# Kernel tuning notes

Hardware: AMD Instinct MI355X
Metric: run time of the kernel (lower is better)

## Reference

```python
import jax, jax.numpy as jnp
import numpy as np

NU, NT, E, H = 100000, 200000, 1000000, 64
NUM_LAYERS = 3


def setup_inputs() -> dict:
    key = jax.random.key(0)
    ks = jax.random.split(key, 16)
    s = 0.05
    inp = {}
    inp["x_user"] = jax.random.normal(ks[0], (NU, 32), jnp.float32)
    inp["x_transaction"] = jax.random.normal(ks[1], (NT, 64), jnp.float32)
    inp["ei_u2u"] = jax.random.randint(ks[2], (2, E), 0, NU, jnp.int32)
    inp["ei_t2t"] = jax.random.randint(ks[3], (2, E), 0, NT, jnp.int32)
    inp["ei_u2t"] = jnp.stack([jax.random.randint(ks[4], (E,), 0, NU),
                               jax.random.randint(ks[5], (E,), 0, NT)]).astype(jnp.int32)
    inp["ei_t2u"] = jnp.stack([jax.random.randint(ks[6], (E,), 0, NT),
                               jax.random.randint(ks[7], (E,), 0, NU)]).astype(jnp.int32)
    inp["W_emb_user"] = jax.random.normal(ks[8], (32, H), jnp.float32) * s
    inp["b_emb_user"] = jnp.zeros((H,), jnp.float32)
    inp["W_emb_txn"] = jax.random.normal(ks[9], (64, H), jnp.float32) * s
    inp["b_emb_txn"] = jnp.zeros((H,), jnp.float32)
    # one GCNConv weight/bias per (layer, edge_type): order u2u, t2t, u2t, t2u
    inp["conv_W"] = jax.random.normal(ks[10], (NUM_LAYERS, 4, H, H), jnp.float32) * s
    inp["conv_b"] = jnp.zeros((NUM_LAYERS, 4, H), jnp.float32)
    inp["W1"] = jax.random.normal(ks[11], (H, H), jnp.float32) * s
    inp["b1"] = jnp.zeros((H,), jnp.float32)
    inp["W2"] = jax.random.normal(ks[12], (H, 1), jnp.float32) * s
    inp["b2"] = jnp.zeros((1,), jnp.float32)
    return inp


def _gcn(h_src, ei, n_src, n_dst, W, b, self_loops):
    """GCNConv: x W with symmetric degree normalization, scatter-sum into dst."""
    src, dst = ei[0], ei[1]
    if self_loops:  # same node type on both ends: add self loops (PyG default)
        loop = jnp.arange(n_dst, dtype=src.dtype)
        src = jnp.concatenate([src, loop])
        dst = jnp.concatenate([dst, loop])
        deg = jax.ops.segment_sum(jnp.ones_like(dst, jnp.float32), dst, num_segments=n_dst)
        dinv = jnp.where(deg > 0, jax.lax.rsqrt(jnp.maximum(deg, 1.0)), 0.0)
        norm = dinv[src] * dinv[dst]
    else:  # bipartite relation: out-degree of src, in-degree of dst
        ds = jax.ops.segment_sum(jnp.ones_like(src, jnp.float32), src, num_segments=n_src)
        dd = jax.ops.segment_sum(jnp.ones_like(dst, jnp.float32), dst, num_segments=n_dst)
        dsi = jnp.where(ds > 0, jax.lax.rsqrt(jnp.maximum(ds, 1.0)), 0.0)
        ddi = jnp.where(dd > 0, jax.lax.rsqrt(jnp.maximum(dd, 1.0)), 0.0)
        norm = dsi[src] * ddi[dst]
    m = h_src @ W  # [N_src, H] transform first (GCNConv order)
    out = jax.ops.segment_sum(m[src] * norm[:, None], dst, num_segments=n_dst)
    return out + b


def reference(x_user, x_transaction, ei_u2u, ei_t2t, ei_u2t, ei_t2u,
              W_emb_user, b_emb_user, W_emb_txn, b_emb_txn,
              conv_W, conv_b, W1, b1, W2, b2):
    hu = x_user @ W_emb_user + b_emb_user          # [NU, H]
    ht = x_transaction @ W_emb_txn + b_emb_txn     # [NT, H]
    for l in range(NUM_LAYERS):
        ou1 = _gcn(hu, ei_u2u, NU, NU, conv_W[l, 0], conv_b[l, 0], True)
        ot1 = _gcn(ht, ei_t2t, NT, NT, conv_W[l, 1], conv_b[l, 1], True)
        ot2 = _gcn(hu, ei_u2t, NU, NT, conv_W[l, 2], conv_b[l, 2], False)
        ou2 = _gcn(ht, ei_t2u, NT, NU, conv_W[l, 3], conv_b[l, 3], False)
        # HeteroConv aggr='mean' across relations per dst type, then ReLU
        hu = jax.nn.relu((ou1 + ou2) * 0.5)
        ht = jax.nn.relu((ot1 + ot2) * 0.5)
    g = jnp.stack([hu.mean(axis=0), ht.mean(axis=0)])  # [2, H] per-type global mean
    x = g.mean(axis=0, keepdims=True)                  # [1, H]
    x = jax.nn.relu(x @ W1 + b1)                       # dropout is identity at eval
    return jax.nn.sigmoid(x @ W2 + b2)                 # [1, 1]
```

## Files before the change

### kernel.cpp

```cpp
#include <hip/hip_runtime.h>
#include <hip/hip_bf16.h>
#include <hip/hip_fp8.h>

#define NU_ 100000
#define NT_ 200000
#define NE_ 1000000
#define HD  64
#define NL  3

#define OFF0 0
#define OFF1 (NU_)
#define OFF2 (NU_ + NT_)
#define OFF3 (NU_ + 2 * NT_)
#define OFF4 (2 * NU_ + 2 * NT_)
#define OFF5 (3 * NU_ + 2 * NT_)
#define HTOT (3 * NU_ + 3 * NT_)
#define RPT2 (NU_ + NT_)

#define NBU 391
#define NBT 782
#define NBTOT2 (NBU + NBT)

#define PB1  512
#define BKP  2048
#define NBKC 147
#define NBKS 147
#define NBKT (NBKC + NBKS)

#define WPK_EMBU 0
#define WPK_EMBT 2048
#define WPK_CONV 6144
#define WPK_TOT  55296

#define EMU 512
#define EMT 1024
#define GMU 512
#define GMT 1024
#define GBU 3125
#define GBT 6250

typedef float floatx2 __attribute__((ext_vector_type(2)));
typedef _Float16 f16x8 __attribute__((ext_vector_type(8)));
typedef float f32x4 __attribute__((ext_vector_type(4)));
typedef unsigned short u16x8 __attribute__((ext_vector_type(8)));

__device__ __forceinline__ unsigned char enc_fp8(float v) {
    return (unsigned char)__hip_cvt_float_to_fp8(v, __HIP_SATFINITE, __HIP_E4M3);
}

__device__ __forceinline__ float dec1_fp8(unsigned int u) {
    int e = (u >> 3) & 15;
    int m = u & 7;
    int mant = m | (e ? 8 : 0);
    if (u & 0x80) mant = -mant;
    int ex = (e ? e : 1) - 10;
    return (float)mant * __uint_as_float((unsigned int)(ex + 127) << 23);
}

__device__ __forceinline__ void dec4_fp8(unsigned int u, float* f) {
#if __has_builtin(__builtin_amdgcn_cvt_pk_f32_fp8)
    floatx2 lo = __builtin_amdgcn_cvt_pk_f32_fp8((int)u, false);
    floatx2 hi = __builtin_amdgcn_cvt_pk_f32_fp8((int)u, true);
    f[0] = lo.x; f[1] = lo.y; f[2] = hi.x; f[3] = hi.y;
#else
    f[0] = dec1_fp8(u & 0xff);
    f[1] = dec1_fp8((u >> 8) & 0xff);
    f[2] = dec1_fp8((u >> 16) & 0xff);
    f[3] = dec1_fp8((u >> 24) & 0xff);
#endif
}

__global__ void detect_dtype(const unsigned short* __restrict__ x, int* __restrict__ flag, int n) {
    __shared__ int s_big;
    if (threadIdx.x == 0) s_big = 0;
    __syncthreads();
    int big = 0;
    for (int i = threadIdx.x; i < n; i += blockDim.x) {
        float v = __uint_as_float(((unsigned int)x[i]) << 16);
        if (!(fabsf(v) < 1.0e4f)) big = 1;
    }
    if (big) atomicAdd(&s_big, 1);
    __syncthreads();
    if (threadIdx.x == 0) flag[0] = (s_big > 0) ? 0 : 1;
}

struct Ptr10 { const void* p[10]; };

__global__ void cvt_weights(Ptr10 src, float* __restrict__ dst, float* __restrict__ gsum,
                            const int* __restrict__ flag) {
    const int c[11] = {0, 2048, 2112, 6208, 6272, 55424, 56192, 60288, 60352, 60416, 60417};
    int i = blockIdx.x * blockDim.x + threadIdx.x;
    if (i < 64) gsum[i] = 0.f;
    if (i >= 60417) return;
    int r = 0;
#pragma unroll
    for (int k = 1; k < 10; ++k)
        if (i >= c[k]) r = k;
    int e = i - c[r];
    if (flag[0]) {
        unsigned short u = ((const unsigned short*)src.p[r])[e];
        dst[i] = __uint_as_float(((unsigned int)u) << 16);
    } else {
        dst[i] = ((const float*)src.p[r])[e];
    }
}

__global__ void pack_weights(const float* __restrict__ wts, _Float16* __restrict__ wpk) {
    int gid = blockIdx.x * 256 + threadIdx.x;
    if (gid >= WPK_TOT) return;
    const float* W;
    int r, KS;
    if (gid < WPK_EMBT) { W = wts; r = gid; KS = 1; }
    else if (gid < WPK_CONV) { W = wts + 2112; r = gid - WPK_EMBT; KS = 2; }
    else {
        int mat = (gid - WPK_CONV) >> 12;
        W = wts + 6272 + mat * 4096;
        r = (gid - WPK_CONV) & 4095;
        KS = 2;
    }
    int j = r & 7;
    int lane = (r >> 3) & 63;
    int f = r >> 9;
    int ct = f / KS;
    int s = f - ct * KS;
    int k = 32 * s + 8 * (lane >> 4) + j;
    int n = 16 * ct + (lane & 15);
    wpk[gid] = (_Float16)W[k * 64 + n];
}

__device__ __forceinline__ void p1_dev(int bid, const int* __restrict__ eu2u,
                                       const int* __restrict__ et2t,
                                       const int* __restrict__ eu2t,
                                       const int* __restrict__ et2u,
                                       int* __restrict__ gcnt, int* __restrict__ bofs) {
    __shared__ int cnt[NBKT];
    for (int j = threadIdx.x; j < NBKT; j += 256) cnt[j] = 0;
    __syncthreads();
    for (int i = bid * 256 + threadIdx.x; i < 6 * NE_; i += PB1 * 256) {
        int b;
        if (i < 4 * NE_) {
            int m;
            if (i < NE_)          m = eu2u[i + NE_];
            else if (i < 2 * NE_) m = NU_ + et2t[i];
            else if (i < 3 * NE_) m = NU_ + eu2t[i - NE_];
            else                  m = et2u[i - 2 * NE_];
            b = m >> 11;
        } else {
            int m2 = (i < 5 * NE_) ? eu2t[i - 4 * NE_] : (NU_ + et2u[i - 5 * NE_]);
            b = NBKC + (m2 >> 11);
        }
        atomicAdd(&cnt[b], 1);
    }
    __syncthreads();
    for (int j = threadIdx.x; j < NBKT; j += 256) {
        bofs[bid * NBKT + j] = atomicAdd(&gcnt[j], cnt[j]);
    }
}

template <int K>
__device__ __forceinline__ void embed_mfma_dev(int t0, int tstride, int ntiles,
                                               const void* __restrict__ x,
                                               const _Float16* __restrict__ Wpk,
                                               const float* __restrict__ bias,
                                               _Float16* __restrict__ out,
                                               const int* __restrict__ flag) {
    constexpr int KS = K / 32;
    const int lane = threadIdx.x & 63;
    const int rq = lane & 15;
    const int oct = lane >> 4;

    f16x8 bf[4][KS];
#pragma unroll
    for (int ct = 0; ct < 4; ++ct)
#pragma unroll
        for (int s = 0; s < KS; ++s)
            bf[ct][s] = *(const f16x8*)(Wpk + (((ct * KS + s) << 9) + (lane << 3)));
    float bv[4];
#pragma unroll
    for (int ct = 0; ct < 4; ++ct) bv[ct] = bias[16 * ct + rq];

    const bool isb = flag[0] != 0;

    for (int t = t0; t < ntiles; t += tstride) {
        const int r0 = t << 4;
        f16x8 a[KS];
        if (isb) {
            const unsigned short* xr = (const unsigned short*)x + (size_t)(r0 + rq) * K + 8 * oct;
#pragma unroll
            for (int s = 0; s < KS; ++s) {
                u16x8 uv = *(const u16x8*)(xr + 32 * s);
                f16x8 v;
#pragma unroll
                for (int j = 0; j < 8; ++j)
                    v[j] = (_Float16)__uint_as_float(((unsigned int)uv[j]) << 16);
                a[s] = v;
            }
        } else {
            const float* xr = (const float*)x + (size_t)(r0 + rq) * K + 8 * oct;
#pragma unroll
            for (int s = 0; s < KS; ++s) {
                float4 x0 = *(const float4*)(xr + 32 * s);
                float4 x1 = *(const float4*)(xr + 32 * s + 4);
                f16x8 v;
                v[0] = (_Float16)x0.x; v[1] = (_Float16)x0.y;
                v[2] = (_Float16)x0.z; v[3] = (_Float16)x0.w;
                v[4] = (_Float16)x1.x; v[5] = (_Float16)x1.y;
                v[6] = (_Float16)x1.z; v[7] = (_Float16)x1.w;
                a[s] = v;
            }
        }

        f32x4 acc[4];
#pragma unroll
        for (int ct = 0; ct < 4; ++ct) acc[ct] = (f32x4){0.f, 0.f, 0.f, 0.f};
#pragma unroll
        for (int ct = 0; ct < 4; ++ct)
#pragma unroll
            for (int s = 0; s < KS; ++s)
                acc[ct] = __builtin_amdgcn_mfma_f32_16x16x32_f16(a[s], bf[ct][s], acc[ct], 0, 0, 0);

        const int rb = r0 + (oct << 2);
#pragma unroll
        for (int ct = 0; ct < 4; ++ct)
#pragma unroll
            for (int g = 0; g < 4; ++g)
                out[(size_t)(rb + g) * HD + 16 * ct + rq] = (_Float16)(acc[ct][g] + bv[ct]);
    }
}

__global__ __launch_bounds__(256) void fused_p1_embed(
    const int* __restrict__ eu2u, const int* __restrict__ et2t,
    const int* __restrict__ eu2t, const int* __restrict__ et2u,
    int* __restrict__ gcnt, int* __restrict__ bofs,
    const void* __restrict__ x_user, const void* __restrict__ x_txn,
    const _Float16* __restrict__ wpk,
    const float* __restrict__ bembu, const float* __restrict__ bembt,
    _Float16* __restrict__ hu, _Float16* __restrict__ ht, const int* __restrict__ flag) {
    int b = blockIdx.x;
    int wid = threadIdx.x >> 6;
    if (b < PB1) {
        p1_dev(b, eu2u, et2t, eu2t, et2u, gcnt, bofs);
    } else if (b < PB1 + EMU) {
        embed_mfma_dev<32>((b - PB1) * 4 + wid, EMU * 4, NU_ / 16, x_user,
                           wpk + WPK_EMBU, bembu, hu, flag);
    } else {
        embed_mfma_dev<64>((b - PB1 - EMU) * 4 + wid, EMT * 4, NT_ / 16, x_txn,
                           wpk + WPK_EMBT, bembt, ht, flag);
    }
}

__global__ __launch_bounds__(256) void p2_scatter(
    const int* __restrict__ eu2u, const int* __restrict__ et2t,
    const int* __restrict__ eu2t, const int* __restrict__ et2u,
    const int* __restrict__ gcnt, int* __restrict__ gbase, const int* __restrict__ bofs,
    unsigned int* __restrict__ part_csr, unsigned int* __restrict__ part_src) {
    __shared__ int gb[NBKT];
    __shared__ int lofs[NBKT];
    const int t = threadIdx.x;
    for (int j = t; j < NBKT; j += 256) { lofs[j] = 0; gb[j] = gcnt[j]; }
    __syncthreads();
    if (t == 0) {
        int s = 0;
        for (int j = 0; j < NBKC; ++j) { int c = gb[j]; gb[j] = s; s += c; }
        s = 0;
        for (int j = NBKC; j < NBKT; ++j) { int c = gb[j]; gb[j] = s; s += c; }
    }
    __syncthreads();
    const int bid = blockIdx.x;
    if (bid == 0)
        for (int j = t; j < NBKT; j += 256) gbase[j] = gb[j];
    for (int i = bid * 256 + t; i < 6 * NE_; i += PB1 * 256) {
        if (i < 4 * NE_) {
            int m; unsigned int src, tag;
            if (i < NE_)          { m = eu2u[i + NE_];        src = (unsigned int)eu2u[i];           tag = 0u; }
            else if (i < 2 * NE_) { m = NU_ + et2t[i];        src = (unsigned int)et2t[i - NE_];     tag = 1u; tag = 0u; }
            else if (i < 3 * NE_) { m = NU_ + eu2t[i - NE_];  src = (unsigned int)eu2t[i - 2 * NE_]; tag = 1u; }
            else                  { m = et2u[i - 2 * NE_];    src = (unsigned int)et2u[i - 3 * NE_]; tag = 1u; }
            int b = m >> 11;
            int l = atomicAdd(&lofs[b], 1);
            int pos = gb[b] + bofs[bid * NBKT + b] + l;
            part_csr[pos] = (src << 12) | (tag << 11) | (unsigned int)(m & (BKP - 1));
        } else {
            int m2 = (i < 5 * NE_) ? eu2t[i - 4 * NE_] : (NU_ + et2u[i - 5 * NE_]);
            int b = NBKC + (m2 >> 11);
            int l = atomicAdd(&lofs[b], 1);
            int pos = gb[b] + bofs[bid * NBKT + b] + l;
            part_src[pos] = (unsigned int)m2;
        }
    }
}

__global__ __launch_bounds__(1024) void bucket_count(const unsigned int* __restrict__ part_csr,
                                                     const unsigned int* __restrict__ part_src,
                                                     const int* __restrict__ gcnt,
                                                     const int* __restrict__ gbase,
                                                     int* __restrict__ hist) {
    __shared__ int cA[BKP];
    __shared__ int cB[BKP];
    const int b = blockIdx.x;
    const int n = gcnt[b];
    const int base = gbase[b];
    const int t = threadIdx.x;
    for (int j = t; j < BKP; j += 1024) { cA[j] = 0; cB[j] = 0; }
    __syncthreads();
    if (b < NBKC) {
        for (int i = t; i < n; i += 1024) {
            unsigned int it = part_csr[base + i];
            int l = (int)(it & (BKP - 1));
            if (it & 0x800u) atomicAdd(&cB[l], 1);
            else             atomicAdd(&cA[l], 1);
        }
        __syncthreads();
        const int m0 = b << 11;
        for (int j = t; j < BKP; j += 1024) {
            int m = m0 + j;
            if (m < NU_ + NT_) {
                int oA = (m < NU_) ? (OFF0 + m) : (OFF1 + (m - NU_));
                int oB = (m < NU_) ? (OFF3 + m) : (OFF2 + (m - NU_));
                hist[oA] = cA[j];
                hist[oB] = cB[j];
            }
        }
    } else {
        for (int i = t; i < n; i += 1024) {
            unsigned int m2 = part_src[base + i];
            atomicAdd(&cA[(int)(m2 & (BKP - 1))], 1);
        }
        __syncthreads();
        const int m0 = (b - NBKC) << 11;
        for (int j = t; j < BKP; j += 1024) {
            int m2 = m0 + j;
            if (m2 < NU_ + NT_) {
                int o = (m2 < NU_) ? (OFF4 + m2) : (OFF5 + (m2 - NU_));
                hist[o] = cA[j];
            }
        }
    }
}

__global__ __launch_bounds__(1024) void bucket_place(const unsigned int* __restrict__ part_csr,
                                                     const int* __restrict__ gcnt,
                                                     const int* __restrict__ gbase,
                                                     const int* __restrict__ rp,
                                                     int* __restrict__ colU,
                                                     int* __restrict__ colT) {
    __shared__ int fl[BKP];
    const int b = blockIdx.x;
    const int n = gcnt[b];
    const int base = gbase[b];
    const int t = threadIdx.x;
    for (int j = t; j < BKP; j += 1024) fl[j] = 0;
    __syncthreads();
    const int m0 = b << 11;
    for (int i = t; i < n; i += 1024) {
        unsigned int it = part_csr[base + i];
        int mlow = (int)(it & (BKP - 1));
        int m = m0 + mlow;
        int ofs = atomicAdd(&fl[mlow], 1);
        int colv = (int)(((it >> 12) << 6) | ((it & 0x800u) << 20));
        if (m < NU_) colU[rp[m] + ofs] = colv;
        else         colT[rp[m] + ofs] = colv;
    }
}

__device__ __forceinline__ void gemm_mfma_dev(int t0, int tstride, int ntiles,
                                              const _Float16* __restrict__ h,
                                              const _Float16* __restrict__ WApk,
                                              const _Float16* __restrict__ WBpk,
                                              const float* __restrict__ scA,
                                              const float* __restrict__ scB,
                                              unsigned char* __restrict__ mA,
                                              unsigned char* __restrict__ mB) {
    const int lane = threadIdx.x & 63;
    const int rq = lane & 15;
    const int oct = lane >> 4;

    f16x8 bf[2][4][2];
#pragma unroll
    for (int m = 0; m < 2; ++m) {
        const _Float16* P = m ? WBpk : WApk;
#pragma unroll
        for (int ct = 0; ct < 4; ++ct)
#pragma unroll
            for (int s = 0; s < 2; ++s)
                bf[m][ct][s] = *(const f16x8*)(P + ((((ct << 1) + s) << 9) + (lane << 3)));
    }

    for (int t = t0; t < ntiles; t += tstride) {
        const int r0 = t << 4;
        const _Float16* hr = h + (size_t)(r0 + rq) * HD + 8 * oct;
        f16x8 a0 = *(const f16x8*)(hr);
        f16x8 a1 = *(const f16x8*)(hr + 32);

        f32x4 acc[2][4];
#pragma unroll
        for (int m = 0; m < 2; ++m)
#pragma unroll
            for (int ct = 0; ct < 4; ++ct) acc[m][ct] = (f32x4){0.f, 0.f, 0.f, 0.f};

#pragma unroll
        for (int m = 0; m < 2; ++m)
#pragma unroll
            for (int ct = 0; ct < 4; ++ct) {
                acc[m][ct] = __builtin_amdgcn_mfma_f32_16x16x32_f16(a0, bf[m][ct][0],
                                                                   acc[m][ct], 0, 0, 0);
                acc[m][ct] = __builtin_amdgcn_mfma_f32_16x16x32_f16(a1, bf[m][ct][1],
                                                                   acc[m][ct], 0, 0, 0);
            }

        const int rb = r0 + (oct << 2);
        float sa[4], sb[4];
#pragma unroll
        for (int g = 0; g < 4; ++g) { sa[g] = scA[rb + g]; sb[g] = scB[rb + g]; }
#pragma unroll
        for (int ct = 0; ct < 4; ++ct)
#pragma unroll
            for (int g = 0; g < 4; ++g) {
                mA[(size_t)(rb + g) * HD + 16 * ct + rq] = enc_fp8(acc[0][ct][g] * sa[g]);
                mB[(size_t)(rb + g) * HD + 16 * ct + rq] = enc_fp8(acc[1][ct][g] * sb[g]);
            }
    }
}

__global__ __launch_bounds__(256) void gemm_dual_both(
    const _Float16* __restrict__ hu, const _Float16* __restrict__ ht,
    const _Float16* __restrict__ W0, const _Float16* __restrict__ Wu2t,
    const _Float16* __restrict__ Wt, const _Float16* __restrict__ Wt2u,
    const float* __restrict__ dinv,
    unsigned char* __restrict__ m_uu, unsigned char* __restrict__ m_ut,
    unsigned char* __restrict__ m_tt, unsigned char* __restrict__ m_tu) {
    int b = blockIdx.x;
    int wid = threadIdx.x >> 6;
    if (b < GMU) {
        gemm_mfma_dev(b * 4 + wid, GMU * 4, NU_ / 16, hu, W0, Wu2t,
                      dinv + OFF0, dinv + OFF4, m_uu, m_ut);
    } else {
        gemm_mfma_dev((b - GMU) * 4 + wid, GMT * 4, NT_ / 16, ht, Wt, Wt2u,
                      dinv + OFF1, dinv + OFF5, m_tt, m_tu);
    }
}

__device__ __forceinline__ void gather_dev(int blk, const unsigned char* __restrict__ msg,
                                           unsigned int offB,
                                           const int4* __restrict__ meta,
                                           const int* __restrict__ col,
                                           const float* __restrict__ ba,
                                           const float* __restrict__ bb,
                                           _Float16* __restrict__ out, int N) {
    const int lane = threadIdx.x & 63;
    const int grp = lane >> 3;
    const int sub = lane & 7;
    const int d = (blk << 5) + ((threadIdx.x >> 6) << 3) + grp;
    const bool valid = d < N;

    int4 mt = make_int4(0, 0, 0, 0);
    if (valid) mt = meta[d];
    const int st = mt.x;
    const int cnt = mt.y;
    const float dA = __int_as_float(mt.z);
    const float dB = __int_as_float(mt.w);
    const unsigned char* msgL = msg + (sub << 3);

    floatx2 acc[4];
#pragma unroll
    for (int q = 0; q < 4; ++q) acc[q] = (floatx2){0.f, 0.f};

    auto consume = [&](uint2 u, float s) {
        floatx2 s2; s2.x = s; s2.y = s;
#if __has_builtin(__builtin_amdgcn_cvt_pk_f32_fp8)
        acc[0] += __builtin_amdgcn_cvt_pk_f32_fp8((int)u.x, false) * s2;
        acc[1] += __builtin_amdgcn_cvt_pk_f32_fp8((int)u.x, true) * s2;
        acc[2] += __builtin_amdgcn_cvt_pk_f32_fp8((int)u.y, false) * s2;
        acc[3] += __builtin_amdgcn_cvt_pk_f32_fp8((int)u.y, true) * s2;
#else
        float f[8];
        dec4_fp8(u.x, f);
        dec4_fp8(u.y, f + 4);
        acc[0].x += f[0] * s; acc[0].y += f[1] * s;
        acc[1].x += f[2] * s; acc[1].y += f[3] * s;
        acc[2].x += f[4] * s; acc[2].y += f[5] * s;
        acc[3].x += f[6] * s; acc[3].y += f[7] * s;
#endif
    };

    if (valid) {
        uint2 uself = *(const uint2*)(msgL + ((unsigned int)d << 6));
        consume(uself, dA);
    }

    int cw = (sub < cnt) ? col[st + sub] : 0;
    int done = 0;
    while (done < cnt) {
        int rem = cnt - done;
        if (rem > 8) rem = 8;

        uint2 ub0, ub1, ub2, ub3, ub4, ub5, ub6, ub7;
        float sc0, sc1, sc2, sc3, sc4, sc5, sc6, sc7;

        auto issue = [&](int p, uint2& ub, float& sc) {
            int c = __shfl(cw, (grp << 3) + p);
            unsigned int off = ((unsigned int)c & 0x7fffffffu) + ((c < 0) ? offB : 0u);
            sc = (p < rem) ? ((c < 0) ? dB : dA) : 0.f;
            ub = *(const uint2*)(msgL + off);
        };

        issue(0, ub0, sc0);
        issue(1, ub1, sc1);
        issue(2, ub2, sc2);
        issue(3, ub3, sc3);
        issue(4, ub4, sc4);
        issue(5, ub5, sc5);
        issue(6, ub6, sc6);
        issue(7, ub7, sc7);

        int nd = done + 8;
        int cw2 = (nd + sub < cnt) ? col[st + nd + sub] : 0;

        consume(ub0, sc0);
        consume(ub1, sc1);
        consume(ub2, sc2);
        consume(ub3, sc3);
        consume(ub4, sc4);
        consume(ub5, sc5);
        consume(ub6, sc6);
        consume(ub7, sc7);

        cw = cw2;
        done = nd;
    }

    if (valid) {
        const int col0 = sub << 3;
        float4 a0 = *(const float4*)(ba + col0);
        float4 a1 = *(const float4*)(ba + col0 + 4);
        float4 c0 = *(const float4*)(bb + col0);
        float4 c1 = *(const float4*)(bb + col0 + 4);
        float af[8] = {acc[0].x, acc[0].y, acc[1].x, acc[1].y,
                       acc[2].x, acc[2].y, acc[3].x, acc[3].y};
        float bf[8] = {a0.x + c0.x, a0.y + c0.y, a0.z + c0.z, a0.w + c0.w,
                       a1.x + c1.x, a1.y + c1.y, a1.z + c1.z, a1.w + c1.w};
        f16x8 o;
#pragma unroll
        for (int k = 0; k < 8; ++k)
            o[k] = (_Float16)fmaxf(af[k] + 0.5f * bf[k], 0.f);
        *(f16x8*)(out + ((size_t)d << 6) + col0) = o;
    }
}

__global__ __launch_bounds__(256) void gather_both(
    const unsigned char* __restrict__ msgU, const unsigned char* __restrict__ msgT,
    const int4* __restrict__ meta,
    const int* __restrict__ colU, const int* __restrict__ colT,
    const float* __restrict__ bU0, const float* __restrict__ bU1,
    const float* __restrict__ bT0, const float* __restrict__ bT1,
    _Float16* __restrict__ hu, _Float16* __restrict__ ht) {
    int b = blockIdx.x;
    if (b < GBU) {
        gather_dev(b, msgU, (unsigned int)NU_ * HD, meta, colU, bU0, bU1, hu, NU_);
    } else {
        gather_dev(b - GBU, msgT, (unsigned int)NT_ * HD, meta + NU_, colT, bT0, bT1, ht, NT_);
    }
}

__global__ __launch_bounds__(256) void scan1m(const int* __restrict__ hist, int* __restrict__ rp,
                                              int* __restrict__ bsums, float* __restrict__ dinv) {
    int b = blockIdx.x, t = threadIdx.x;
    int r, lb, n, rpbase, oA, oB;
    if (b < NBU) { r = 0; lb = b;       n = NU_; rpbase = 0;   oA = OFF0; oB = OFF3; }
    else         { r = 1; lb = b - NBU; n = NT_; rpbase = NU_; oA = OFF1; oB = OFF2; }
    int i = lb * 256 + t;
    int hA = (i < n) ? hist[oA + i] : 0;
    int hB = (i < n) ? hist[oB + i] : 0;
    if (i < n) {
        dinv[oA + i] = rsqrtf((float)hA + 1.0f);
        dinv[oB + i] = (hB > 0) ? rsqrtf((float)hB) : 0.f;
    }
    int v = hA + hB;
    __shared__ int s[256];
    s[t] = v;
    __syncthreads();
    for (int off = 1; off < 256; off <<= 1) {
        int x = (t >= off) ? s[t - off] : 0;
        __syncthreads();
        s[t] += x;
        __syncthreads();
    }
    if (i < n) rp[rpbase + i] = s[t] - v;
    if (t == 255) bsums[r * 1024 + lb] = s[255];
}

__global__ __launch_bounds__(1024) void scan2m(int* __restrict__ bsums) {
    int r = blockIdx.x, t = threadIdx.x;
    const int nb = r ? NBT : NBU;
    int v = (t < nb) ? bsums[r * 1024 + t] : 0;
    __shared__ int s[1024];
    s[t] = v;
    __syncthreads();
    for (int off = 1; off < 1024; off <<= 1) {
        int x = (t >= off) ? s[t - off] : 0;
        __syncthreads();
        s[t] += x;
        __syncthreads();
    }
    if (t < nb) bsums[r * 1024 + t] = s[t] - v;
}

__global__ void scan3m(int* __restrict__ rp, const int* __restrict__ bsums,
                       const int* __restrict__ hist, float* __restrict__ dinv,
                       int4* __restrict__ meta) {
    int gid = blockIdx.x * blockDim.x + threadIdx.x;
    if (gid >= RPT2) return;
    int r = (gid < NU_) ? 0 : 1;
    int base = r ? NU_ : 0;
    int lb = (gid - base) >> 8;
    int rpf = rp[gid] + bsums[r * 1024 + lb];
    rp[gid] = rpf;
    int si = r ? (OFF5 + gid - NU_) : (OFF4 + gid);
    int h = hist[si];
    dinv[si] = (h > 0) ? rsqrtf((float)h) : 0.f;
    int oA = r ? (OFF1 + gid - NU_) : (OFF0 + gid);
    int oB = r ? (OFF2 + gid - NU_) : (OFF3 + gid);
    int hA = hist[oA];
    int hB = hist[oB];
    float dA = 0.5f * rsqrtf((float)hA + 1.0f);
    float dB = (hB > 0) ? 0.5f * rsqrtf((float)hB) : 0.f;
    int4 mt;
    mt.x = rpf;
    mt.y = hA + hB;
    mt.z = __float_as_int(dA);
    mt.w = __float_as_int(dB);
    meta[gid] = mt;
}

__global__ __launch_bounds__(256) void colmean_both(const _Float16* __restrict__ hu,
                                                    const _Float16* __restrict__ ht,
                                                    float* __restrict__ gsum) {
    const bool isU = blockIdx.x < 512;
    const _Float16* h = isU ? hu : ht;
    const int n = isU ? NU_ : NT_;
    const float scale = isU ? 0.5f / NU_ : 0.5f / NT_;
    const int blk = isU ? blockIdx.x : blockIdx.x - 512;
    const int lane = threadIdx.x & 63;
    const int w = threadIdx.x >> 6;
    float s = 0.f;
    for (int r = blk * 4 + w; r < n; r += 512 * 4)
        s += (float)h[(size_t)r * HD + lane];
    __shared__ float red[256];
    red[threadIdx.x] = s;
    __syncthreads();
    if (threadIdx.x < 64) {
        float t = red[threadIdx.x] + red[64 + threadIdx.x] + red[128 + threadIdx.x] +
                  red[192 + threadIdx.x];
        atomicAdd(&gsum[lane], t * scale);
    }
}

__global__ void head(const float* __restrict__ g, const float* __restrict__ W1,
                     const float* __restrict__ b1, const float* __restrict__ W2,
                     const float* __restrict__ b2, const int* __restrict__ flag,
                     void* __restrict__ out) {
    const int c = threadIdx.x;
    float x = b1[c];
    for (int k = 0; k < HD; ++k) x = fmaf(g[k], W1[k * HD + c], x);
    x = fmaxf(x, 0.f);
    float t = x * W2[c];
    for (int off = 32; off; off >>= 1) t += __shfl_down(t, off);
    if (c == 0) {
        float z = t + b2[0];
        float s = 1.f / (1.f + expf(-z));
        if (flag[0]) *(__hip_bfloat16*)out = __float2bfloat16(s);
        else *(float*)out = s;
    }
}

extern "C" void kernel_launch(void* const* d_in, const int* in_sizes, int n_in,
                              void* d_out, int out_size, void* d_ws, size_t ws_size,
                              hipStream_t stream) {
    const void* x_user = d_in[0];
    const void* x_txn  = d_in[1];
    const int* ei_u2u = (const int*)d_in[2];
    const int* ei_t2t = (const int*)d_in[3];
    const int* ei_u2t = (const int*)d_in[4];
    const int* ei_t2u = (const int*)d_in[5];

    float* ws = (float*)d_ws;
    _Float16* hu = (_Float16*)ws;
    _Float16* ht = hu + (size_t)NU_ * HD;
    float* dinv = (float*)(ht + (size_t)NT_ * HD);
    float* wts = dinv + HTOT;
    float* gsum = wts + 60432;
    _Float16* wpk = (_Float16*)(gsum + 64);
    unsigned char* m_uu = (unsigned char*)(wpk + WPK_TOT);
    unsigned char* m_tu = m_uu + (size_t)NU_ * HD;
    unsigned char* m_tt = m_tu + (size_t)NT_ * HD;
    unsigned char* m_ut = m_tt + (size_t)NT_ * HD;
    int* hist = (int*)(m_ut + (size_t)NU_ * HD);
    int* aux  = hist + HTOT;
    int* rp   = aux + RPT2;
    int* bsums = rp + RPT2;
    int* colU = bsums + 2048;
    int* colT = colU + 2 * NE_;
    int4* meta = (int4*)(colT + 2 * NE_);
    int* dflag = (int*)(meta + RPT2);

    int* gcnt  = aux;
    int* gbase = gcnt + NBKT;
    int* bofs  = gbase + NBKT;

    unsigned int* part_csr = (unsigned int*)m_uu;
    unsigned int* part_src = (unsigned int*)colU;

    float* bembu = wts + 2048;
    float* bembt = wts + 6208;
    float* convbf = wts + 55424;
    float* W1f = wts + 56192;
    float* b1f = W1f + 4096;
    float* W2f = b1f + 64;
    float* b2f = W2f + 64;

    hipMemsetAsync(gcnt, 0, (size_t)NBKT * sizeof(int), stream);

    detect_dtype<<<1, 256, 0, stream>>>((const unsigned short*)x_user, dflag, 2048);
    {
        Ptr10 p;
        for (int k = 0; k < 10; ++k) p.p[k] = d_in[6 + k];
        cvt_weights<<<(60417 + 255) / 256, 256, 0, stream>>>(p, wts, gsum, dflag);
    }
    pack_weights<<<(WPK_TOT + 255) / 256, 256, 0, stream>>>(wts, wpk);

    fused_p1_embed<<<PB1 + EMU + EMT, 256, 0, stream>>>(
        ei_u2u, ei_t2t, ei_u2t, ei_t2u, gcnt, bofs,
        x_user, x_txn, wpk, bembu, bembt, hu, ht, dflag);

    p2_scatter<<<PB1, 256, 0, stream>>>(ei_u2u, ei_t2t, ei_u2t, ei_t2u,
                                        gcnt, gbase, bofs, part_csr, part_src);
    bucket_count<<<NBKT, 1024, 0, stream>>>(part_csr, part_src, gcnt, gbase, hist);

    scan1m<<<NBTOT2, 256, 0, stream>>>(hist, rp, bsums, dinv);
    scan2m<<<2, 1024, 0, stream>>>(bsums);
    scan3m<<<(RPT2 + 255) / 256, 256, 0, stream>>>(rp, bsums, hist, dinv, meta);

    bucket_place<<<NBKC, 1024, 0, stream>>>(part_csr, gcnt, gbase, rp, colU, colT);

    for (int l = 0; l < NL; ++l) {
        const _Float16* W0   = wpk + WPK_CONV + ((size_t)l * 4 + 0) * 4096;
        const _Float16* Wt   = wpk + WPK_CONV + ((size_t)l * 4 + 1) * 4096;
        const _Float16* Wu2t = wpk + WPK_CONV + ((size_t)l * 4 + 2) * 4096;
        const _Float16* Wt2u = wpk + WPK_CONV + ((size_t)l * 4 + 3) * 4096;
        const float* B0   = convbf + ((size_t)l * 4 + 0) * HD;
        const float* Bt   = convbf + ((size_t)l * 4 + 1) * HD;
        const float* Bu2t = convbf + ((size_t)l * 4 + 2) * HD;
        const float* Bt2u = convbf + ((size_t)l * 4 + 3) * HD;

        gemm_dual_both<<<GMU + GMT, 256, 0, stream>>>(hu, ht, W0, Wu2t, Wt, Wt2u, dinv,
                                                      m_uu, m_ut, m_tt, m_tu);

        gather_both<<<GBU + GBT, 256, 0, stream>>>(m_uu, m_tt,
                                                   meta, colU, colT,
                                                   B0, Bt2u, Bt, Bu2t, hu, ht);
    }

    colmean_both<<<1024, 256, 0, stream>>>(hu, ht, gsum);
    head<<<1, 64, 0, stream>>>(gsum, W1f, b1f, W2f, b2f, dflag, d_out);
}
```

Measured before the change: 610.4 us.

## Fold embedding into layer-0 conv weights and merge CSR build kernels

```diff
diff --git a/kernel.cpp b/kernel.cpp
--- a/kernel.cpp
+++ b/kernel.cpp
@@ -10,16 +10,10 @@
 
 #define OFF0 0
 #define OFF1 (NU_)
-#define OFF2 (NU_ + NT_)
-#define OFF3 (NU_ + 2 * NT_)
 #define OFF4 (2 * NU_ + 2 * NT_)
 #define OFF5 (3 * NU_ + 2 * NT_)
 #define HTOT (3 * NU_ + 3 * NT_)
 #define RPT2 (NU_ + NT_)
-
-#define NBU 391
-#define NBT 782
-#define NBTOT2 (NBU + NBT)
 
 #define PB1  512
 #define BKP  2048
@@ -30,10 +24,12 @@
 #define WPK_EMBU 0
 #define WPK_EMBT 2048
 #define WPK_CONV 6144
-#define WPK_TOT  55296
-
-#define EMU 512
-#define EMT 1024
+#define WPK_G0U  55296
+#define WPK_G0T  59392
+#define WPK_TOT  67584
+#define PK_ELEMS (WPK_TOT + 256)
+#define PKB      ((PK_ELEMS + 255) / 256)
+
 #define GMU 512
 #define GMT 1024
 #define GBU 3125
@@ -105,27 +101,70 @@
     }
 }
 
-__global__ void pack_weights(const float* __restrict__ wts, _Float16* __restrict__ wpk) {
-    int gid = blockIdx.x * 256 + threadIdx.x;
-    if (gid >= WPK_TOT) return;
-    const float* W;
-    int r, KS;
-    if (gid < WPK_EMBT) { W = wts; r = gid; KS = 1; }
-    else if (gid < WPK_CONV) { W = wts + 2112; r = gid - WPK_EMBT; KS = 2; }
-    else {
-        int mat = (gid - WPK_CONV) >> 12;
-        W = wts + 6272 + mat * 4096;
-        r = (gid - WPK_CONV) & 4095;
-        KS = 2;
-    }
-    int j = r & 7;
-    int lane = (r >> 3) & 63;
-    int f = r >> 9;
-    int ct = f / KS;
-    int s = f - ct * KS;
-    int k = 32 * s + 8 * (lane >> 4) + j;
-    int n = 16 * ct + (lane & 15);
-    wpk[gid] = (_Float16)W[k * 64 + n];
+__device__ __forceinline__ void pack_dev(int gid, const float* __restrict__ wts,
+                                         _Float16* __restrict__ wpk,
+                                         float* __restrict__ bcomp) {
+    if (gid >= PK_ELEMS) return;
+    if (gid < WPK_G0U) {
+        const float* W;
+        int r, KS;
+        if (gid < WPK_EMBT) { W = wts; r = gid; KS = 1; }
+        else if (gid < WPK_CONV) { W = wts + 2112; r = gid - WPK_EMBT; KS = 2; }
+        else {
+            int mat = (gid - WPK_CONV) >> 12;
+            W = wts + 6272 + mat * 4096;
+            r = (gid - WPK_CONV) & 4095;
+            KS = 2;
+        }
+        int j = r & 7;
+        int lane = (r >> 3) & 63;
+        int f = r >> 9;
+        int ct = f / KS;
+        int s = f - ct * KS;
+        int k = 32 * s + 8 * (lane >> 4) + j;
+        int n = 16 * ct + (lane & 15);
+        wpk[gid] = (_Float16)W[k * 64 + n];
+    } else if (gid < WPK_TOT) {
+        const float* We;
+        int matc, rr, KS;
+        if (gid < WPK_G0T) {
+            int r = gid - WPK_G0U;
+            matc = (r >> 11) ? 2 : 0;
+            rr = r & 2047;
+            We = wts;
+            KS = 1;
+        } else {
+            int r = gid - WPK_G0T;
+            matc = (r >> 12) ? 3 : 1;
+            rr = r & 4095;
+            We = wts + 2112;
+            KS = 2;
+        }
+        const float* Wc = wts + 6272 + matc * 4096;
+        int j = rr & 7;
+        int lane = (rr >> 3) & 63;
+        int f = rr >> 9;
+        int ct = f / KS;
+        int s = f - ct * KS;
+        int k = 32 * s + 8 * (lane >> 4) + j;
+        int n = 16 * ct + (lane & 15);
+        float acc = 0.f;
+#pragma unroll
+        for (int q = 0; q < 64; ++q)
+            acc = fmaf(We[k * 64 + q], Wc[q * 64 + n], acc);
+        wpk[gid] = (_Float16)acc;
+    } else {
+        int q = gid - WPK_TOT;
+        int mat = q >> 6;
+        int n = q & 63;
+        const float* be = (mat == 0 || mat == 2) ? (wts + 2048) : (wts + 6208);
+        const float* Wc = wts + 6272 + mat * 4096;
+        float acc = 0.f;
+#pragma unroll
+        for (int k = 0; k < 64; ++k)
+            acc = fmaf(be[k], Wc[k * 64 + n], acc);
+        bcomp[q] = acc;
+    }
 }
 
 __device__ __forceinline__ void p1_dev(int bid, const int* __restrict__ eu2u,
@@ -157,95 +196,16 @@
     }
 }
 
-template <int K>
-__device__ __forceinline__ void embed_mfma_dev(int t0, int tstride, int ntiles,
-                                               const void* __restrict__ x,
-                                               const _Float16* __restrict__ Wpk,
-                                               const float* __restrict__ bias,
-                                               _Float16* __restrict__ out,
-                                               const int* __restrict__ flag) {
-    constexpr int KS = K / 32;
-    const int lane = threadIdx.x & 63;
-    const int rq = lane & 15;
-    const int oct = lane >> 4;
-
-    f16x8 bf[4][KS];
-#pragma unroll
-    for (int ct = 0; ct < 4; ++ct)
-#pragma unroll
-        for (int s = 0; s < KS; ++s)
-            bf[ct][s] = *(const f16x8*)(Wpk + (((ct * KS + s) << 9) + (lane << 3)));
-    float bv[4];
-#pragma unroll
-    for (int ct = 0; ct < 4; ++ct) bv[ct] = bias[16 * ct + rq];
-
-    const bool isb = flag[0] != 0;
-
-    for (int t = t0; t < ntiles; t += tstride) {
-        const int r0 = t << 4;
-        f16x8 a[KS];
-        if (isb) {
-            const unsigned short* xr = (const unsigned short*)x + (size_t)(r0 + rq) * K + 8 * oct;
-#pragma unroll
-            for (int s = 0; s < KS; ++s) {
-                u16x8 uv = *(const u16x8*)(xr + 32 * s);
-                f16x8 v;
-#pragma unroll
-                for (int j = 0; j < 8; ++j)
-                    v[j] = (_Float16)__uint_as_float(((unsigned int)uv[j]) << 16);
-                a[s] = v;
-            }
-        } else {
-            const float* xr = (const float*)x + (size_t)(r0 + rq) * K + 8 * oct;
-#pragma unroll
-            for (int s = 0; s < KS; ++s) {
-                float4 x0 = *(const float4*)(xr + 32 * s);
-                float4 x1 = *(const float4*)(xr + 32 * s + 4);
-                f16x8 v;
-                v[0] = (_Float16)x0.x; v[1] = (_Float16)x0.y;
-                v[2] = (_Float16)x0.z; v[3] = (_Float16)x0.w;
-                v[4] = (_Float16)x1.x; v[5] = (_Float16)x1.y;
-                v[6] = (_Float16)x1.z; v[7] = (_Float16)x1.w;
-                a[s] = v;
-            }
-        }
-
-        f32x4 acc[4];
-#pragma unroll
-        for (int ct = 0; ct < 4; ++ct) acc[ct] = (f32x4){0.f, 0.f, 0.f, 0.f};
-#pragma unroll
-        for (int ct = 0; ct < 4; ++ct)
-#pragma unroll
-            for (int s = 0; s < KS; ++s)
-                acc[ct] = __builtin_amdgcn_mfma_f32_16x16x32_f16(a[s], bf[ct][s], acc[ct], 0, 0, 0);
-
-        const int rb = r0 + (oct << 2);
-#pragma unroll
-        for (int ct = 0; ct < 4; ++ct)
-#pragma unroll
-            for (int g = 0; g < 4; ++g)
-                out[(size_t)(rb + g) * HD + 16 * ct + rq] = (_Float16)(acc[ct][g] + bv[ct]);
-    }
-}
-
-__global__ __launch_bounds__(256) void fused_p1_embed(
+__global__ __launch_bounds__(256) void fused_p1_pack(
     const int* __restrict__ eu2u, const int* __restrict__ et2t,
     const int* __restrict__ eu2t, const int* __restrict__ et2u,
     int* __restrict__ gcnt, int* __restrict__ bofs,
-    const void* __restrict__ x_user, const void* __restrict__ x_txn,
-    const _Float16* __restrict__ wpk,
-    const float* __restrict__ bembu, const float* __restrict__ bembt,
-    _Float16* __restrict__ hu, _Float16* __restrict__ ht, const int* __restrict__ flag) {
+    const float* __restrict__ wts, _Float16* __restrict__ wpk, float* __restrict__ bcomp) {
     int b = blockIdx.x;
-    int wid = threadIdx.x >> 6;
     if (b < PB1) {
         p1_dev(b, eu2u, et2t, eu2t, et2u, gcnt, bofs);
-    } else if (b < PB1 + EMU) {
-        embed_mfma_dev<32>((b - PB1) * 4 + wid, EMU * 4, NU_ / 16, x_user,
-                           wpk + WPK_EMBU, bembu, hu, flag);
     } else {
-        embed_mfma_dev<64>((b - PB1 - EMU) * 4 + wid, EMT * 4, NT_ / 16, x_txn,
-                           wpk + WPK_EMBT, bembt, ht, flag);
+        pack_dev((b - PB1) * 256 + threadIdx.x, wts, wpk, bcomp);
     }
 }
 
@@ -273,7 +233,7 @@
         if (i < 4 * NE_) {
             int m; unsigned int src, tag;
             if (i < NE_)          { m = eu2u[i + NE_];        src = (unsigned int)eu2u[i];           tag = 0u; }
-            else if (i < 2 * NE_) { m = NU_ + et2t[i];        src = (unsigned int)et2t[i - NE_];     tag = 1u; tag = 0u; }
+            else if (i < 2 * NE_) { m = NU_ + et2t[i];        src = (unsigned int)et2t[i - NE_];     tag = 0u; }
             else if (i < 3 * NE_) { m = NU_ + eu2t[i - NE_];  src = (unsigned int)eu2t[i - 2 * NE_]; tag = 1u; }
             else                  { m = et2u[i - 2 * NE_];    src = (unsigned int)et2u[i - 3 * NE_]; tag = 1u; }
             int b = m >> 11;
@@ -290,76 +250,207 @@
     }
 }
 
-__global__ __launch_bounds__(1024) void bucket_count(const unsigned int* __restrict__ part_csr,
-                                                     const unsigned int* __restrict__ part_src,
-                                                     const int* __restrict__ gcnt,
-                                                     const int* __restrict__ gbase,
-                                                     int* __restrict__ hist) {
-    __shared__ int cA[BKP];
-    __shared__ int cB[BKP];
+__global__ __launch_bounds__(1024) void bucket_build(
+    const unsigned int* __restrict__ part_csr, const unsigned int* __restrict__ part_src,
+    const int* __restrict__ gcnt, const int* __restrict__ gbase,
+    float* __restrict__ dinv, int4* __restrict__ meta,
+    int* __restrict__ colU, int* __restrict__ colT) {
     const int b = blockIdx.x;
-    const int n = gcnt[b];
-    const int base = gbase[b];
     const int t = threadIdx.x;
-    for (int j = t; j < BKP; j += 1024) { cA[j] = 0; cB[j] = 0; }
-    __syncthreads();
-    if (b < NBKC) {
-        for (int i = t; i < n; i += 1024) {
-            unsigned int it = part_csr[base + i];
-            int l = (int)(it & (BKP - 1));
-            if (it & 0x800u) atomicAdd(&cB[l], 1);
-            else             atomicAdd(&cA[l], 1);
-        }
+    if (b >= NBKC) {
+        __shared__ int cS[BKP];
+        const int n = gcnt[b];
+        const int base = gbase[b];
+        for (int j = t; j < BKP; j += 1024) cS[j] = 0;
         __syncthreads();
-        const int m0 = b << 11;
-        for (int j = t; j < BKP; j += 1024) {
-            int m = m0 + j;
-            if (m < NU_ + NT_) {
-                int oA = (m < NU_) ? (OFF0 + m) : (OFF1 + (m - NU_));
-                int oB = (m < NU_) ? (OFF3 + m) : (OFF2 + (m - NU_));
-                hist[oA] = cA[j];
-                hist[oB] = cB[j];
-            }
-        }
-    } else {
-        for (int i = t; i < n; i += 1024) {
-            unsigned int m2 = part_src[base + i];
-            atomicAdd(&cA[(int)(m2 & (BKP - 1))], 1);
-        }
+        for (int i = t; i < n; i += 1024)
+            atomicAdd(&cS[(int)(part_src[base + i] & (BKP - 1))], 1);
         __syncthreads();
         const int m0 = (b - NBKC) << 11;
         for (int j = t; j < BKP; j += 1024) {
             int m2 = m0 + j;
             if (m2 < NU_ + NT_) {
                 int o = (m2 < NU_) ? (OFF4 + m2) : (OFF5 + (m2 - NU_));
-                hist[o] = cA[j];
+                int h = cS[j];
+                dinv[o] = (h > 0) ? rsqrtf((float)h) : 0.f;
             }
         }
-    }
-}
-
-__global__ __launch_bounds__(1024) void bucket_place(const unsigned int* __restrict__ part_csr,
-                                                     const int* __restrict__ gcnt,
-                                                     const int* __restrict__ gbase,
-                                                     const int* __restrict__ rp,
-                                                     int* __restrict__ colU,
-                                                     int* __restrict__ colT) {
-    __shared__ int fl[BKP];
-    const int b = blockIdx.x;
+        return;
+    }
+    __shared__ int cA[BKP];
+    __shared__ int cB[BKP];
+    __shared__ int lp[BKP];
+    __shared__ int s1[1024];
     const int n = gcnt[b];
     const int base = gbase[b];
-    const int t = threadIdx.x;
-    for (int j = t; j < BKP; j += 1024) fl[j] = 0;
+    for (int j = t; j < BKP; j += 1024) { cA[j] = 0; cB[j] = 0; }
+    __syncthreads();
+    for (int i = t; i < n; i += 1024) {
+        unsigned int it = part_csr[base + i];
+        int l = (int)(it & (BKP - 1));
+        if (it & 0x800u) atomicAdd(&cB[l], 1);
+        else             atomicAdd(&cA[l], 1);
+    }
+    __syncthreads();
+    const int j0 = t << 1, j1 = j0 + 1;
+    const int a0 = cA[j0] + cB[j0];
+    const int a1 = cA[j1] + cB[j1];
+    const int ps = a0 + a1;
+    s1[t] = ps;
+    __syncthreads();
+    for (int off = 1; off < 1024; off <<= 1) {
+        int x = (t >= off) ? s1[t - off] : 0;
+        __syncthreads();
+        s1[t] += x;
+        __syncthreads();
+    }
+    const int excl = s1[t] - ps;
+    lp[j0] = excl;
+    lp[j1] = excl + a0;
     __syncthreads();
     const int m0 = b << 11;
+    const int gb0 = gbase[b];
+    for (int j = t; j < BKP; j += 1024) {
+        int m = m0 + j;
+        if (m < NU_ + NT_) {
+            int hA = cA[j], hB = cB[j];
+            float dslf = rsqrtf((float)hA + 1.0f);
+            int oA = (m < NU_) ? (OFF0 + m) : (OFF1 + (m - NU_));
+            dinv[oA] = dslf;
+            int4 mt;
+            mt.x = gb0 + lp[j] - ((m >= NU_) ? 2 * NE_ : 0);
+            mt.y = hA + hB;
+            mt.z = __float_as_int(0.5f * dslf);
+            mt.w = __float_as_int((hB > 0) ? 0.5f * rsqrtf((float)hB) : 0.f);
+            meta[m] = mt;
+        }
+    }
+    __syncthreads();
+    for (int j = t; j < BKP; j += 1024) cA[j] = 0;
+    __syncthreads();
     for (int i = t; i < n; i += 1024) {
         unsigned int it = part_csr[base + i];
         int mlow = (int)(it & (BKP - 1));
+        int ofs = atomicAdd(&cA[mlow], 1);
+        int g = gb0 + lp[mlow] + ofs;
+        int colv = (int)(((it >> 12) << 6) | ((it & 0x800u) << 20));
         int m = m0 + mlow;
-        int ofs = atomicAdd(&fl[mlow], 1);
-        int colv = (int)(((it >> 12) << 6) | ((it & 0x800u) << 20));
-        if (m < NU_) colU[rp[m] + ofs] = colv;
-        else         colT[rp[m] + ofs] = colv;
+        if (m < NU_) colU[g] = colv;
+        else         colT[g - 2 * NE_] = colv;
+    }
+}
+
+template <int K>
+__device__ __forceinline__ void gemm0_dev(int t0, int tstride, int ntiles,
+                                          const void* __restrict__ x,
+                                          const _Float16* __restrict__ WApk,
+                                          const _Float16* __restrict__ WBpk,
+                                          const float* __restrict__ bA,
+                                          const float* __restrict__ bB,
+                                          const float* __restrict__ scA,
+                                          const float* __restrict__ scB,
+                                          unsigned char* __restrict__ mA,
+                                          unsigned char* __restrict__ mB,
+                                          const int* __restrict__ flag) {
+    constexpr int KS = K / 32;
+    const int lane = threadIdx.x & 63;
+    const int rq = lane & 15;
+    const int oct = lane >> 4;
+
+    f16x8 bf[2][4][KS];
+#pragma unroll
+    for (int m = 0; m < 2; ++m) {
+        const _Float16* P = m ? WBpk : WApk;
+#pragma unroll
+        for (int ct = 0; ct < 4; ++ct)
+#pragma unroll
+            for (int s = 0; s < KS; ++s)
+                bf[m][ct][s] = *(const f16x8*)(P + (((ct * KS + s) << 9) + (lane << 3)));
+    }
+    float bvA[4], bvB[4];
+#pragma unroll
+    for (int ct = 0; ct < 4; ++ct) { bvA[ct] = bA[16 * ct + rq]; bvB[ct] = bB[16 * ct + rq]; }
+
+    const bool isb = flag[0] != 0;
+
+    for (int t = t0; t < ntiles; t += tstride) {
+        const int r0 = t << 4;
+        f16x8 a[KS];
+        if (isb) {
+            const unsigned short* xr = (const unsigned short*)x + (size_t)(r0 + rq) * K + 8 * oct;
+#pragma unroll
+            for (int s = 0; s < KS; ++s) {
+                u16x8 uv = *(const u16x8*)(xr + 32 * s);
+                f16x8 v;
+#pragma unroll
+                for (int j = 0; j < 8; ++j)
+                    v[j] = (_Float16)__uint_as_float(((unsigned int)uv[j]) << 16);
+                a[s] = v;
+            }
+        } else {
+            const float* xr = (const float*)x + (size_t)(r0 + rq) * K + 8 * oct;
+#pragma unroll
+            for (int s = 0; s < KS; ++s) {
+                float4 x0 = *(const float4*)(xr + 32 * s);
+                float4 x1 = *(const float4*)(xr + 32 * s + 4);
+                f16x8 v;
+                v[0] = (_Float16)x0.x; v[1] = (_Float16)x0.y;
+                v[2] = (_Float16)x0.z; v[3] = (_Float16)x0.w;
+                v[4] = (_Float16)x1.x; v[5] = (_Float16)x1.y;
+                v[6] = (_Float16)x1.z; v[7] = (_Float16)x1.w;
+                a[s] = v;
+            }
+        }
+
+        f32x4 acc[2][4];
+#pragma unroll
+        for (int m = 0; m < 2; ++m)
+#pragma unroll
+            for (int ct = 0; ct < 4; ++ct) acc[m][ct] = (f32x4){0.f, 0.f, 0.f, 0.f};
+#pragma unroll
+        for (int m = 0; m < 2; ++m)
+#pragma unroll
+            for (int ct = 0; ct < 4; ++ct)
+#pragma unroll
+                for (int s = 0; s < KS; ++s)
+                    acc[m][ct] = __builtin_amdgcn_mfma_f32_16x16x32_f16(a[s], bf[m][ct][s],
+                                                                       acc[m][ct], 0, 0, 0);
+
+        const int rb = r0 + (oct << 2);
+        float sa[4], sb[4];
+#pragma unroll
+        for (int g = 0; g < 4; ++g) { sa[g] = scA[rb + g]; sb[g] = scB[rb + g]; }
+#pragma unroll
+        for (int ct = 0; ct < 4; ++ct)
+#pragma unroll
+            for (int g = 0; g < 4; ++g) {
+                mA[(size_t)(rb + g) * HD + 16 * ct + rq] =
+                    enc_fp8((acc[0][ct][g] + bvA[ct]) * sa[g]);
+                mB[(size_t)(rb + g) * HD + 16 * ct + rq] =
+                    enc_fp8((acc[1][ct][g] + bvB[ct]) * sb[g]);
+            }
+    }
+}
+
+__global__ __launch_bounds__(256) void gemm0_both(
+    const void* __restrict__ x_user, const void* __restrict__ x_txn,
+    const _Float16* __restrict__ wpk, const float* __restrict__ bcomp,
+    const float* __restrict__ dinv,
+    unsigned char* __restrict__ m_uu, unsigned char* __restrict__ m_ut,
+    unsigned char* __restrict__ m_tt, unsigned char* __restrict__ m_tu,
+    const int* __restrict__ flag) {
+    int b = blockIdx.x;
+    int wid = threadIdx.x >> 6;
+    if (b < GMU) {
+        gemm0_dev<32>(b * 4 + wid, GMU * 4, NU_ / 16, x_user,
+                      wpk + WPK_G0U, wpk + WPK_G0U + 2048,
+                      bcomp + 0, bcomp + 128,
+                      dinv + OFF0, dinv + OFF4, m_uu, m_ut, flag);
+    } else {
+        gemm0_dev<64>((b - GMU) * 4 + wid, GMT * 4, NT_ / 16, x_txn,
+                      wpk + WPK_G0T, wpk + WPK_G0T + 4096,
+                      bcomp + 64, bcomp + 192,
+                      dinv + OFF1, dinv + OFF5, m_tt, m_tu, flag);
     }
 }
 
@@ -562,76 +653,6 @@
     }
 }
 
-__global__ __launch_bounds__(256) void scan1m(const int* __restrict__ hist, int* __restrict__ rp,
-                                              int* __restrict__ bsums, float* __restrict__ dinv) {
-    int b = blockIdx.x, t = threadIdx.x;
-    int r, lb, n, rpbase, oA, oB;
-    if (b < NBU) { r = 0; lb = b;       n = NU_; rpbase = 0;   oA = OFF0; oB = OFF3; }
-    else         { r = 1; lb = b - NBU; n = NT_; rpbase = NU_; oA = OFF1; oB = OFF2; }
-    int i = lb * 256 + t;
-    int hA = (i < n) ? hist[oA + i] : 0;
-    int hB = (i < n) ? hist[oB + i] : 0;
-    if (i < n) {
-        dinv[oA + i] = rsqrtf((float)hA + 1.0f);
-        dinv[oB + i] = (hB > 0) ? rsqrtf((float)hB) : 0.f;
-    }
-    int v = hA + hB;
-    __shared__ int s[256];
-    s[t] = v;
-    __syncthreads();
-    for (int off = 1; off < 256; off <<= 1) {
-        int x = (t >= off) ? s[t - off] : 0;
-        __syncthreads();
-        s[t] += x;
-        __syncthreads();
-    }
-    if (i < n) rp[rpbase + i] = s[t] - v;
-    if (t == 255) bsums[r * 1024 + lb] = s[255];
-}
-
-__global__ __launch_bounds__(1024) void scan2m(int* __restrict__ bsums) {
-    int r = blockIdx.x, t = threadIdx.x;
-    const int nb = r ? NBT : NBU;
-    int v = (t < nb) ? bsums[r * 1024 + t] : 0;
-    __shared__ int s[1024];
-    s[t] = v;
-    __syncthreads();
-    for (int off = 1; off < 1024; off <<= 1) {
-        int x = (t >= off) ? s[t - off] : 0;
-        __syncthreads();
-        s[t] += x;
-        __syncthreads();
-    }
-    if (t < nb) bsums[r * 1024 + t] = s[t] - v;
-}
-
-__global__ void scan3m(int* __restrict__ rp, const int* __restrict__ bsums,
-                       const int* __restrict__ hist, float* __restrict__ dinv,
-                       int4* __restrict__ meta) {
-    int gid = blockIdx.x * blockDim.x + threadIdx.x;
-    if (gid >= RPT2) return;
-    int r = (gid < NU_) ? 0 : 1;
-    int base = r ? NU_ : 0;
-    int lb = (gid - base) >> 8;
-    int rpf = rp[gid] + bsums[r * 1024 + lb];
-    rp[gid] = rpf;
-    int si = r ? (OFF5 + gid - NU_) : (OFF4 + gid);
-    int h = hist[si];
-    dinv[si] = (h > 0) ? rsqrtf((float)h) : 0.f;
-    int oA = r ? (OFF1 + gid - NU_) : (OFF0 + gid);
-    int oB = r ? (OFF2 + gid - NU_) : (OFF3 + gid);
-    int hA = hist[oA];
-    int hB = hist[oB];
-    float dA = 0.5f * rsqrtf((float)hA + 1.0f);
-    float dB = (hB > 0) ? 0.5f * rsqrtf((float)hB) : 0.f;
-    int4 mt;
-    mt.x = rpf;
-    mt.y = hA + hB;
-    mt.z = __float_as_int(dA);
-    mt.w = __float_as_int(dB);
-    meta[gid] = mt;
-}
-
 __global__ __launch_bounds__(256) void colmean_both(const _Float16* __restrict__ hu,
                                                     const _Float16* __restrict__ ht,
                                                     float* __restrict__ gsum) {
@@ -689,16 +710,14 @@
     float* dinv = (float*)(ht + (size_t)NT_ * HD);
     float* wts = dinv + HTOT;
     float* gsum = wts + 60432;
-    _Float16* wpk = (_Float16*)(gsum + 64);
+    float* bcomp = gsum + 64;
+    _Float16* wpk = (_Float16*)(bcomp + 256);
     unsigned char* m_uu = (unsigned char*)(wpk + WPK_TOT);
     unsigned char* m_tu = m_uu + (size_t)NU_ * HD;
     unsigned char* m_tt = m_tu + (size_t)NT_ * HD;
     unsigned char* m_ut = m_tt + (size_t)NT_ * HD;
-    int* hist = (int*)(m_ut + (size_t)NU_ * HD);
-    int* aux  = hist + HTOT;
-    int* rp   = aux + RPT2;
-    int* bsums = rp + RPT2;
-    int* colU = bsums + 2048;
+    int* aux  = (int*)(m_ut + (size_t)NU_ * HD);
+    int* colU = aux + 2 * NBKT + PB1 * NBKT;
     int* colT = colU + 2 * NE_;
     int4* meta = (int4*)(colT + 2 * NE_);
     int* dflag = (int*)(meta + RPT2);
@@ -708,11 +727,8 @@
     int* bofs  = gbase + NBKT;
 
     unsigned int* part_csr = (unsigned int*)m_uu;
-    unsigned int* part_src = (unsigned int*)colU;
-
-    float* bembu = wts + 2048;
-    float* bembt = wts + 6208;
-    float* convbf = wts + 55424;
+    unsigned int* part_src = (unsigned int*)hu;
+
     float* W1f = wts + 56192;
     float* b1f = W1f + 4096;
     float* W2f = b1f + 64;
@@ -726,34 +742,34 @@
         for (int k = 0; k < 10; ++k) p.p[k] = d_in[6 + k];
         cvt_weights<<<(60417 + 255) / 256, 256, 0, stream>>>(p, wts, gsum, dflag);
     }
-    pack_weights<<<(WPK_TOT + 255) / 256, 256, 0, stream>>>(wts, wpk);
-
-    fused_p1_embed<<<PB1 + EMU + EMT, 256, 0, stream>>>(
-        ei_u2u, ei_t2t, ei_u2t, ei_t2u, gcnt, bofs,
-        x_user, x_txn, wpk, bembu, bembt, hu, ht, dflag);
+
+    fused_p1_pack<<<PB1 + PKB, 256, 0, stream>>>(ei_u2u, ei_t2t, ei_u2t, ei_t2u,
+                                                 gcnt, bofs, wts, wpk, bcomp);
 
     p2_scatter<<<PB1, 256, 0, stream>>>(ei_u2u, ei_t2t, ei_u2t, ei_t2u,
                                         gcnt, gbase, bofs, part_csr, part_src);
-    bucket_count<<<NBKT, 1024, 0, stream>>>(part_csr, part_src, gcnt, gbase, hist);
-
-    scan1m<<<NBTOT2, 256, 0, stream>>>(hist, rp, bsums, dinv);
-    scan2m<<<2, 1024, 0, stream>>>(bsums);
-    scan3m<<<(RPT2 + 255) / 256, 256, 0, stream>>>(rp, bsums, hist, dinv, meta);
-
-    bucket_place<<<NBKC, 1024, 0, stream>>>(part_csr, gcnt, gbase, rp, colU, colT);
+
+    bucket_build<<<NBKT, 1024, 0, stream>>>(part_csr, part_src, gcnt, gbase,
+                                            dinv, meta, colU, colT);
 
     for (int l = 0; l < NL; ++l) {
-        const _Float16* W0   = wpk + WPK_CONV + ((size_t)l * 4 + 0) * 4096;
-        const _Float16* Wt   = wpk + WPK_CONV + ((size_t)l * 4 + 1) * 4096;
-        const _Float16* Wu2t = wpk + WPK_CONV + ((size_t)l * 4 + 2) * 4096;
-        const _Float16* Wt2u = wpk + WPK_CONV + ((size_t)l * 4 + 3) * 4096;
+        const float* convbf = wts + 55424;
         const float* B0   = convbf + ((size_t)l * 4 + 0) * HD;
         const float* Bt   = convbf + ((size_t)l * 4 + 1) * HD;
         const float* Bu2t = convbf + ((size_t)l * 4 + 2) * HD;
         const float* Bt2u = convbf + ((size_t)l * 4 + 3) * HD;
 
-        gemm_dual_both<<<GMU + GMT, 256, 0, stream>>>(hu, ht, W0, Wu2t, Wt, Wt2u, dinv,
-                                                      m_uu, m_ut, m_tt, m_tu);
+        if (l == 0) {
+            gemm0_both<<<GMU + GMT, 256, 0, stream>>>(x_user, x_txn, wpk, bcomp, dinv,
+                                                      m_uu, m_ut, m_tt, m_tu, dflag);
+        } else {
+            const _Float16* W0   = wpk + WPK_CONV + ((size_t)l * 4 + 0) * 4096;
+            const _Float16* Wt   = wpk + WPK_CONV + ((size_t)l * 4 + 1) * 4096;
+            const _Float16* Wu2t = wpk + WPK_CONV + ((size_t)l * 4 + 2) * 4096;
+            const _Float16* Wt2u = wpk + WPK_CONV + ((size_t)l * 4 + 3) * 4096;
+            gemm_dual_both<<<GMU + GMT, 256, 0, stream>>>(hu, ht, W0, Wu2t, Wt, Wt2u, dinv,
+                                                          m_uu, m_ut, m_tt, m_tu);
+        }
 
         gather_both<<<GBU + GBT, 256, 0, stream>>>(m_uu, m_tt,
                                                    meta, colU, colT,
```

Measured after the change: 582.5 us. -4.6%, faster.
